# Kernel optimization log

Measured on AMD Instinct MI355X. Metric: run time of the kernel, lower is better.

The kernel has to match this reference:

```python
import jax, jax.numpy as jnp
import numpy as np

B, C, N, H = 4, 512, 2048, 8
D = C // H  # per-head depth = 64
EPS = 1e-5


def conv1x1(x, W, b):
    # x: [B, Cin, N], W: [Cout, Cin], b: [Cout]
    return jnp.einsum('oc,bcn->bon', W, x) + b[None, :, None]


def instance_norm(x):
    # normalize over length dim per (batch, channel), no affine
    mu = jnp.mean(x, axis=-1, keepdims=True)
    var = jnp.var(x, axis=-1, keepdims=True)
    return (x - mu) * jax.lax.rsqrt(var + EPS)


def _pipeline(src, tgt, Wq, bq, Wk, bk, Wv, bv, Wm, bm):
    # query from src, key/value from tgt; reshape C -> (D outer, H inner)
    q = conv1x1(src, Wq, bq).reshape(B, D, H, N)
    k = conv1x1(tgt, Wk, bk).reshape(B, D, H, N)
    v = conv1x1(tgt, Wv, bv).reshape(B, D, H, N)
    scores = jnp.einsum('bdhn,bdhm->bhnm', q, k) / jnp.sqrt(jnp.float32(D))
    probs = jax.nn.softmax(scores, axis=-1)
    out = jnp.einsum('bhnm,bdhm->bdhn', probs, v).reshape(B, C, N)
    return conv1x1(out, Wm, bm)


def _mlp(x, W1, b1, W2, b2):
    h = conv1x1(x, W1, b1)
    h = jax.nn.relu(instance_norm(h))
    return conv1x1(h, W2, b2)


def setup_inputs() -> dict:
    key = jax.random.key(0)
    ks = jax.random.split(key, 8)
    s = 0.02
    return {
        'source_features': jax.random.normal(ks[0], (B, C, N), jnp.float32),
        'target_features': jax.random.normal(ks[1], (B, C, N), jnp.float32),
        'Wq': jax.random.normal(ks[2], (C, C), jnp.float32) * s,
        'bq': jnp.zeros((C,), jnp.float32),
        'Wk': jax.random.normal(ks[3], (C, C), jnp.float32) * s,
        'bk': jnp.zeros((C,), jnp.float32),
        'Wv': jax.random.normal(ks[4], (C, C), jnp.float32) * s,
        'bv': jnp.zeros((C,), jnp.float32),
        'Wm': jax.random.normal(ks[5], (C, C), jnp.float32) * s,
        'bm': jnp.zeros((C,), jnp.float32),
        'W1': jax.random.normal(ks[6], (2 * C, 2 * C), jnp.float32) * s,
        'b1': jnp.zeros((2 * C,), jnp.float32),
        'W2': jax.random.normal(ks[7], (C, 2 * C), jnp.float32) * s,
        'b2': jnp.zeros((C,), jnp.float32),
    }


def reference(source_features, target_features, Wq, bq, Wk, bk, Wv, bv, Wm, bm, W1, b1, W2, b2):
    src, tgt = source_features, target_features
    # source update uses ORIGINAL target features
    src_att = _pipeline(src, tgt, Wq, bq, Wk, bk, Wv, bv, Wm, bm)
    src = src + _mlp(jnp.concatenate([src, src_att], axis=1), W1, b1, W2, b2)
    # target update uses the UPDATED source features (in-place semantics of original)
    tgt_att = _pipeline(tgt, src, Wq, bq, Wk, bk, Wv, bv, Wm, bm)
    tgt = tgt + _mlp(jnp.concatenate([tgt, tgt_att], axis=1), W1, b1, W2, b2)
    return src, tgt
```

## Files before the change

### kernel.cpp

```cpp
#include <hip/hip_runtime.h>

#define NN 2048
#define CC 512
#define BB 4
#define HH 8
#define DD 64
#define SCALE 0.18033688011112043f

typedef unsigned short u16;
typedef __attribute__((ext_vector_type(8))) short bf16x8;
typedef __attribute__((ext_vector_type(4))) float f32x4;

extern "C" __device__ float __ocml_native_exp2_f32(float);

__device__ inline u16 f2b(float x) {
    unsigned u = __builtin_bit_cast(unsigned, x);
    u += 0x7fffu + ((u >> 16) & 1u);
    return (u16)(u >> 16);
}
__device__ inline float b2f(u16 h) {
    unsigned u = ((unsigned)h) << 16;
    return __builtin_bit_cast(float, u);
}

#define GLD16(g, l) __builtin_amdgcn_global_load_lds( \
    (const __attribute__((address_space(1))) unsigned int*)(g), \
    (__attribute__((address_space(3))) unsigned int*)(l), 16, 0, 0)

template<int JT, bool DBUF>
__device__ __forceinline__ void gemm_core_t(
    const u16* __restrict__ Xa, const u16* __restrict__ Xb, int Ca, int K,
    const u16* __restrict__ Wt, size_t rowBase,
    u16* As, u16* Bs, f32x4 (&acc)[4][JT])
{
    constexpr int OT = JT * 32;
    constexpr int ASZ = 128 * 64, BSZ = OT * 64;
    const int tid = threadIdx.x;
    const int lane = tid & 63, w = tid >> 6;
    const int quad = lane >> 4, l16 = lane & 15;
    const int wrow = w & 1, wcol = w >> 1;
    const int arow = lane >> 3, aseg = lane & 7;
    const int asw = aseg ^ arow;
    const int lk = l16 & 7;

    auto stage = [&](int k0, u16* Ad, u16* Bd) {
        const u16* Xs; int Crow, cc;
        if (k0 < Ca) { Xs = Xa; Crow = Ca; cc = k0; }
        else         { Xs = Xb; Crow = K - Ca; cc = k0 - Ca; }
#pragma unroll
        for (int i = 0; i < 4; ++i) {
            int rl = w * 32 + i * 8 + arow;
            int la = __builtin_amdgcn_readfirstlane((w * 32 + i * 8) * 64);
            GLD16(Xs + (rowBase + rl) * (size_t)Crow + cc + asw * 8, (char*)Ad + (size_t)la * 2);
        }
#pragma unroll
        for (int i = 0; i < OT / 32; ++i) {
            int rl = w * (OT / 4) + i * 8 + arow;
            int la = __builtin_amdgcn_readfirstlane((w * (OT / 4) + i * 8) * 64);
            GLD16(Wt + (size_t)rl * K + k0 + asw * 8, (char*)Bd + (size_t)la * 2);
        }
    };
    auto compute = [&](const u16* Ac, const u16* Bc) {
#pragma unroll
        for (int kk = 0; kk < 2; ++kk) {
            const int g = ((kk * 4 + quad) ^ lk) * 8;
            bf16x8 av[4], bv[JT];
#pragma unroll
            for (int i = 0; i < 4; ++i)
                av[i] = *(const bf16x8*)&Ac[(wrow * 64 + i * 16 + l16) * 64 + g];
#pragma unroll
            for (int jj = 0; jj < JT; ++jj)
                bv[jj] = *(const bf16x8*)&Bc[(wcol * JT * 16 + jj * 16 + l16) * 64 + g];
#pragma unroll
            for (int i = 0; i < 4; ++i)
#pragma unroll
                for (int jj = 0; jj < JT; ++jj)
                    acc[i][jj] = __builtin_amdgcn_mfma_f32_16x16x32_bf16(av[i], bv[jj], acc[i][jj], 0, 0, 0);
        }
    };

    if constexpr (DBUF) {
        stage(0, As, Bs);
        const int nt = K / 64;
        for (int t = 0; t < nt; ++t) {
            const u16* Ac = As + (t & 1) * ASZ;
            const u16* Bc = Bs + (t & 1) * BSZ;
            __syncthreads();
            if (t + 1 < nt)
                stage((t + 1) * 64, As + ((t + 1) & 1) * ASZ, Bs + ((t + 1) & 1) * BSZ);
            compute(Ac, Bc);
        }
    } else {
        for (int k0 = 0; k0 < K; k0 += 64) {
            stage(k0, As, Bs);
            __syncthreads();
            compute(As, Bs);
            __syncthreads();
        }
    }
}

template<int JT>
__device__ __forceinline__ void gemm_epilogue_t(
    f32x4 (&acc)[4][JT], const float* __restrict__ bias, int mode,
    int b, int n0, int o0, int Cout,
    const float* __restrict__ res, float* __restrict__ outF, u16* __restrict__ outB)
{
    const int tid = threadIdx.x;
    const int lane = tid & 63, w = tid >> 6;
    const int quad = lane >> 4, l16 = lane & 15;
    const int wrow = w & 1, wcol = w >> 1;
    const size_t bN = (size_t)b * NN;
    const int nb0 = n0 + wrow * 64, ob0 = o0 + wcol * JT * 16;

    if (mode == 0) {
#pragma unroll
        for (int j = 0; j < JT; ++j) {
            int o = ob0 + j * 16 + l16;
            float bs = bias[o];
#pragma unroll
            for (int i = 0; i < 4; ++i)
#pragma unroll
                for (int r = 0; r < 4; ++r) {
                    int n = nb0 + i * 16 + quad * 4 + r;
                    outB[(bN + n) * Cout + o] = f2b(acc[i][j][r] + bs);
                }
        }
    } else if (mode == 1) {
#pragma unroll
        for (int j = 0; j < JT; ++j) {
            int o = ob0 + j * 16 + l16;
            float bs = bias[o];
            int h = o >> 6, d = o & 63;
#pragma unroll
            for (int i = 0; i < 4; ++i) {
                int n = nb0 + i * 16 + quad * 4;
                ushort4 pk;
                pk.x = f2b(acc[i][j][0] + bs); pk.y = f2b(acc[i][j][1] + bs);
                pk.z = f2b(acc[i][j][2] + bs); pk.w = f2b(acc[i][j][3] + bs);
                *(ushort4*)&outB[(((size_t)b * HH + h) * DD + d) * NN + n] = pk;
            }
        }
    } else {
#pragma unroll
        for (int j = 0; j < JT; ++j) {
            int o = ob0 + j * 16 + l16;
            float bs = bias[o];
#pragma unroll
            for (int i = 0; i < 4; ++i) {
                int n = nb0 + i * 16 + quad * 4;
                size_t ad = ((size_t)b * Cout + o) * NN + n;
                float4 rv = *(const float4*)&res[ad];
                float4 yv;
                yv.x = acc[i][j][0] + bs + rv.x;
                yv.y = acc[i][j][1] + bs + rv.y;
                yv.z = acc[i][j][2] + bs + rv.z;
                yv.w = acc[i][j][3] + bs + rv.w;
                *(float4*)&outF[ad] = yv;
                if (mode == 2) {
                    outB[(bN + n + 0) * Cout + o] = f2b(yv.x);
                    outB[(bN + n + 1) * Cout + o] = f2b(yv.y);
                    outB[(bN + n + 2) * Cout + o] = f2b(yv.z);
                    outB[(bN + n + 3) * Cout + o] = f2b(yv.w);
                }
            }
        }
    }
}

template<int JT>
__global__ __launch_bounds__(256, (JT == 2 ? 3 : 2)) void gemm_bf16_t(
    const u16* __restrict__ Wb, const float* __restrict__ bias,
    const u16* __restrict__ Xa, const u16* __restrict__ Xb,
    int Ca, int K, int Cout,
    const float* __restrict__ res, float* __restrict__ outF,
    u16* __restrict__ outB, int mode)
{
    __shared__ u16 As[2 * 128 * 64];
    __shared__ u16 Bs[2 * JT * 32 * 64];
    const int b = blockIdx.z, n0 = blockIdx.x * 128, o0 = blockIdx.y * (JT * 32);
    f32x4 acc[4][JT] = {};
    gemm_core_t<JT, true>(Xa, Xb, Ca, K, Wb + (size_t)o0 * K, (size_t)b * NN + n0, As, Bs, acc);
    gemm_epilogue_t<JT>(acc, bias, mode, b, n0, o0, Cout, res, outF, outB);
}

__global__ __launch_bounds__(256, 3) void gemm_qkv(
    const u16* __restrict__ WQ, const float* __restrict__ bQ,
    const u16* __restrict__ XQ, u16* __restrict__ outQ,
    const u16* __restrict__ WK, const float* __restrict__ bK, u16* __restrict__ outK,
    const u16* __restrict__ WV, const float* __restrict__ bV, u16* __restrict__ outV,
    const u16* __restrict__ XKV)
{
    __shared__ u16 As[128 * 64];
    __shared__ u16 Bs[128 * 64];
    const int yb = blockIdx.y;
    const u16* W; const float* bias; const u16* X; u16* outB; int mode, o0;
    if (yb < 4)      { o0 = yb * 128;       W = WQ; bias = bQ; X = XQ;  outB = outQ; mode = 0; }
    else if (yb < 8) { o0 = (yb - 4) * 128; W = WK; bias = bK; X = XKV; outB = outK; mode = 0; }
    else             { o0 = (yb - 8) * 128; W = WV; bias = bV; X = XKV; outB = outV; mode = 1; }
    const int b = blockIdx.z, n0 = blockIdx.x * 128;
    f32x4 acc[4][4] = {};
    gemm_core_t<4, false>(X, nullptr, 512, 512, W + (size_t)o0 * 512, (size_t)b * NN + n0, As, Bs, acc);
    gemm_epilogue_t<4>(acc, bias, mode, b, n0, o0, 512, nullptr, nullptr, outB);
}

__global__ __launch_bounds__(512, 4) void attn(
    const u16* __restrict__ Qg, const u16* __restrict__ Kg,
    const u16* __restrict__ Vg, u16* __restrict__ Og)
{
    __shared__ __align__(16) u16 pool[6 * 4096];
    u16* const Ksb[2] = { pool, pool + 4096 };
    u16* const Vtb[2] = { pool + 2 * 4096, pool + 3 * 4096 };
    u16* const Ps = pool + 4 * 4096;
    const int tid = threadIdx.x;
    const int lane = tid & 63, w = tid >> 6;
    const int qg = w & 3, hv = w >> 2;
    const int quad = lane >> 4, l16 = lane & 15;
    const int id = blockIdx.x;
    const int xcd = id & 7, jj = id >> 3;
    const int bh = xcd * 4 + (jj >> 4), nb = jj & 15;
    const int b = bh >> 3, h = bh & 7;
    const int n0 = nb * 128, wn0 = qg * 32;
    const int sr0 = w * 8;
    const size_t qkBase = ((size_t)b * NN) * CC + h * DD;
    const size_t vBase  = (((size_t)b * HH + h) * DD) * NN;
    const int r8 = lane >> 3, seg = lane & 7;
    const int segp = seg ^ r8;
    const int lk = l16 & 7;

    const u16* kp = Kg + qkBase + (size_t)(sr0 + r8) * CC + segp * 8;
    const u16* vp = Vg + vBase + (size_t)(sr0 + r8) * NN + segp * 8;

    bf16x8 qf[2][2];
#pragma unroll
    for (int qs = 0; qs < 2; ++qs) {
        int n = n0 + wn0 + qs * 16 + l16;
#pragma unroll
        for (int ks = 0; ks < 2; ++ks)
            qf[qs][ks] = *(const bf16x8*)&Qg[qkBase + (size_t)n * CC + ks * 32 + quad * 8];
    }

    const short oneb = 0x3F80;
    const bf16x8 ones = {oneb, oneb, oneb, oneb, oneb, oneb, oneb, oneb};
    f32x4 oa[2][4] = {};
    f32x4 lacc[2] = {};

    GLD16(kp, Ksb[0] + sr0 * 64);
    GLD16(vp, Vtb[0] + sr0 * 64);
    kp += 64 * CC; vp += 64;

#define ATTN_PREF(BUF) do { \
        GLD16(kp, Ksb[BUF] + sr0 * 64); \
        GLD16(vp, Vtb[BUF] + sr0 * 64); \
        kp += 64 * CC; vp += 64; \
    } while (0)

#define ATTN_BODY(CUR) do { \
        const u16* ksb = Ksb[CUR]; \
        const u16* vtb = Vtb[CUR]; \
        f32x4 st[2][2] = {}; \
        _Pragma("unroll") \
        for (int ks = 0; ks < 2; ++ks) { \
            bf16x8 ak[2]; \
            _Pragma("unroll") \
            for (int rtl = 0; rtl < 2; ++rtl) \
                ak[rtl] = *(const bf16x8*)&ksb[(hv * 32 + rtl * 16 + l16) * 64 + ((ks * 4 + quad) ^ lk) * 8]; \
            __builtin_amdgcn_s_setprio(1); \
            _Pragma("unroll") \
            for (int rtl = 0; rtl < 2; ++rtl) \
                _Pragma("unroll") \
                for (int qs = 0; qs < 2; ++qs) \
                    st[qs][rtl] = __builtin_amdgcn_mfma_f32_16x16x32_bf16(ak[rtl], qf[qs][ks], st[qs][rtl], 0, 0, 0); \
            __builtin_amdgcn_s_setprio(0); \
        } \
        _Pragma("unroll") \
        for (int qs = 0; qs < 2; ++qs) { \
            int nrow = wn0 + qs * 16 + l16; \
            _Pragma("unroll") \
            for (int rtl = 0; rtl < 2; ++rtl) { \
                unsigned u0 = __builtin_bit_cast(unsigned, __ocml_native_exp2_f32(st[qs][rtl][0])); \
                unsigned u1 = __builtin_bit_cast(unsigned, __ocml_native_exp2_f32(st[qs][rtl][1])); \
                unsigned u2 = __builtin_bit_cast(unsigned, __ocml_native_exp2_f32(st[qs][rtl][2])); \
                unsigned u3 = __builtin_bit_cast(unsigned, __ocml_native_exp2_f32(st[qs][rtl][3])); \
                uint2 t; \
                t.x = __builtin_amdgcn_perm(u1, u0, 0x07060302u); \
                t.y = __builtin_amdgcn_perm(u3, u2, 0x07060302u); \
                int g = (((hv * 2 + rtl) * 2 + (quad >> 1))) ^ lk; \
                *(uint2*)&Ps[nrow * 64 + g * 8 + (quad & 1) * 4] = t; \
            } \
        } \
        { \
            bf16x8 pa[2]; \
            _Pragma("unroll") \
            for (int qs = 0; qs < 2; ++qs) \
                pa[qs] = *(const bf16x8*)&Ps[(wn0 + qs * 16 + l16) * 64 + ((hv * 4 + quad) ^ lk) * 8]; \
            bf16x8 vb[4]; \
            _Pragma("unroll") \
            for (int ct = 0; ct < 4; ++ct) \
                vb[ct] = *(const bf16x8*)&vtb[(ct * 16 + l16) * 64 + ((hv * 4 + quad) ^ lk) * 8]; \
            __builtin_amdgcn_s_setprio(1); \
            _Pragma("unroll") \
            for (int ct = 0; ct < 4; ++ct) \
                _Pragma("unroll") \
                for (int qs = 0; qs < 2; ++qs) \
                    oa[qs][ct] = __builtin_amdgcn_mfma_f32_16x16x32_bf16(pa[qs], vb[ct], oa[qs][ct], 0, 0, 0); \
            _Pragma("unroll") \
            for (int qs = 0; qs < 2; ++qs) \
                lacc[qs] = __builtin_amdgcn_mfma_f32_16x16x32_bf16(pa[qs], ones, lacc[qs], 0, 0, 0); \
            __builtin_amdgcn_s_setprio(0); \
        } \
    } while (0)

    for (int it = 0; it < NN / 64; it += 2) {
        __syncthreads();
        ATTN_PREF(1);
        ATTN_BODY(0);
        __syncthreads();
        if (it < NN / 64 - 2)
            ATTN_PREF(0);
        ATTN_BODY(1);
    }
#undef ATTN_PREF
#undef ATTN_BODY

    __syncthreads();
    float* M = (float*)pool;
    const int mbase = (qg * 64 + lane) * 41;
    if (hv == 1) {
#pragma unroll
        for (int qs = 0; qs < 2; ++qs)
#pragma unroll
            for (int ct = 0; ct < 4; ++ct)
                *(f32x4*)&M[mbase + (qs * 4 + ct) * 4] = oa[qs][ct];
        *(f32x4*)&M[mbase + 32] = lacc[0];
        *(f32x4*)&M[mbase + 36] = lacc[1];
    }
    __syncthreads();
    if (hv == 0) {
#pragma unroll
        for (int qs = 0; qs < 2; ++qs)
#pragma unroll
            for (int ct = 0; ct < 4; ++ct)
                oa[qs][ct] += *(const f32x4*)&M[mbase + (qs * 4 + ct) * 4];
        lacc[0] += *(const f32x4*)&M[mbase + 32];
        lacc[1] += *(const f32x4*)&M[mbase + 36];
#pragma unroll
        for (int qs = 0; qs < 2; ++qs)
#pragma unroll
            for (int r = 0; r < 4; ++r) {
                float li = 1.f / lacc[qs][r];
                int n = n0 + wn0 + qs * 16 + quad * 4 + r;
#pragma unroll
                for (int ct = 0; ct < 4; ++ct)
                    Og[qkBase + (size_t)n * CC + ct * 16 + l16] = f2b(oa[qs][ct][r] * li);
            }
    }
}

__global__ __launch_bounds__(256) void transpose_cvt(
    const float* __restrict__ X, u16* __restrict__ Y)
{
    __shared__ float T[64][65];
    const int tid = threadIdx.x;
    const int n0 = blockIdx.x * 64, c0 = blockIdx.y * 64, b = blockIdx.z;
    const int rr = tid >> 4, cc4 = tid & 15;
#pragma unroll
    for (int p = 0; p < 4; ++p) {
        int cl = p * 16 + rr;
        float4 v = *(const float4*)&X[((size_t)b * CC + c0 + cl) * NN + n0 + cc4 * 4];
        T[cl][cc4 * 4 + 0] = v.x; T[cl][cc4 * 4 + 1] = v.y;
        T[cl][cc4 * 4 + 2] = v.z; T[cl][cc4 * 4 + 3] = v.w;
    }
    __syncthreads();
#pragma unroll
    for (int p = 0; p < 4; ++p) {
        int nl = p * 16 + rr;
        ushort4 pk;
        pk.x = f2b(T[cc4 * 4 + 0][nl]);
        pk.y = f2b(T[cc4 * 4 + 1][nl]);
        pk.z = f2b(T[cc4 * 4 + 2][nl]);
        pk.w = f2b(T[cc4 * 4 + 3][nl]);
        *(ushort4*)&Y[((size_t)b * NN + n0 + nl) * CC + c0 + cc4 * 4] = pk;
    }
}

__global__ __launch_bounds__(256) void prep_weights(
    const float* __restrict__ Wq, const float* __restrict__ Wk,
    const float* __restrict__ Wv, const float* __restrict__ Wm,
    const float* __restrict__ W1, const float* __restrict__ W2,
    u16* oQ, u16* oK, u16* oV, u16* oM, u16* o1, u16* o2)
{
    const float* W; u16* o; int rows, cols, perm; float sc = 1.f;
    switch (blockIdx.z) {
        case 0: W = Wq; o = oQ; rows = 512;  cols = 512;  perm = 1; sc = SCALE; break;
        case 1: W = Wk; o = oK; rows = 512;  cols = 512;  perm = 1; break;
        case 2: W = Wv; o = oV; rows = 512;  cols = 512;  perm = 1; break;
        case 3: W = Wm; o = oM; rows = 512;  cols = 512;  perm = 2; break;
        case 4: W = W1; o = o1; rows = 1024; cols = 1024; perm = 0; break;
        default: W = W2; o = o2; rows = 512; cols = 1024; perm = 0; break;
    }
    int c = blockIdx.x * 256 + threadIdx.x;
    int r = blockIdx.y;
    if (r >= rows || c >= cols) return;
    int sr = r, scol = c;
    if (perm == 1) sr = (r & 63) * 8 + (r >> 6);
    else if (perm == 2) scol = (c & 63) * 8 + (c >> 6);
    o[(size_t)r * cols + c] = f2b(W[(size_t)sr * cols + scol] * sc);
}

__global__ void prep_bias(const float* __restrict__ bq, const float* __restrict__ bk,
                          const float* __restrict__ bv,
                          float* oq, float* ok, float* ov)
{
    int i = blockIdx.x * 256 + threadIdx.x;
    int y = blockIdx.y;
    const float* s = (y == 0) ? bq : (y == 1) ? bk : bv;
    float* o = (y == 0) ? oq : (y == 1) ? ok : ov;
    float v = s[(i & 63) * 8 + (i >> 6)];
    if (y == 0) v *= SCALE;
    o[i] = v;
}

__global__ __launch_bounds__(256) void inorm_p1(
    const u16* __restrict__ X, float* __restrict__ Ssum, float* __restrict__ Ssq)
{
    __shared__ float rs[4][64], rq[4][64];
    const int tid = threadIdx.x;
    const int cl = tid & 63, g = tid >> 6;
    const int c = blockIdx.x * 64 + cl;
    const int b = blockIdx.y, nz = blockIdx.z;
    float s = 0.f, q = 0.f;
    size_t base = ((size_t)b * NN + nz * 256 + g * 64) * 1024 + c;
#pragma unroll 4
    for (int i = 0; i < 64; ++i) {
        float x = b2f(X[base + (size_t)i * 1024]);
        s += x; q += x * x;
    }
    rs[g][cl] = s; rq[g][cl] = q;
    __syncthreads();
    if (g == 0) {
        s = rs[0][cl] + rs[1][cl] + rs[2][cl] + rs[3][cl];
        q = rq[0][cl] + rq[1][cl] + rq[2][cl] + rq[3][cl];
        atomicAdd(&Ssum[b * 1024 + c], s);
        atomicAdd(&Ssq[b * 1024 + c], q);
    }
}

__global__ __launch_bounds__(256) void inorm_p2(
    u16* __restrict__ X, const float* __restrict__ Ssum, const float* __restrict__ Ssq)
{
    const int tid = threadIdx.x;
    const int cl = tid & 63, g = tid >> 6;
    const int c = blockIdx.x * 64 + cl;
    const int b = blockIdx.y, nz = blockIdx.z;
    float mean = Ssum[b * 1024 + c] * (1.f / NN);
    float var  = Ssq[b * 1024 + c] * (1.f / NN) - mean * mean;
    float rstd = rsqrtf(fmaxf(var, 0.f) + 1e-5f);
    size_t base = ((size_t)b * NN + nz * 256 + g * 64) * 1024 + c;
#pragma unroll 4
    for (int i = 0; i < 64; ++i) {
        float x = b2f(X[base + (size_t)i * 1024]);
        x = (x - mean) * rstd;
        X[base + (size_t)i * 1024] = f2b(fmaxf(x, 0.f));
    }
}

extern "C" void kernel_launch(void* const* d_in, const int* in_sizes, int n_in,
                              void* d_out, int out_size, void* d_ws, size_t ws_size,
                              hipStream_t stream)
{
    (void)in_sizes; (void)n_in; (void)out_size; (void)ws_size;
    const float* src = (const float*)d_in[0];
    const float* tgt = (const float*)d_in[1];
    const float* Wq = (const float*)d_in[2];  const float* bq = (const float*)d_in[3];
    const float* Wk = (const float*)d_in[4];  const float* bk = (const float*)d_in[5];
    const float* Wv = (const float*)d_in[6];  const float* bv = (const float*)d_in[7];
    const float* Wm = (const float*)d_in[8];  const float* bm = (const float*)d_in[9];
    const float* W1 = (const float*)d_in[10]; const float* b1 = (const float*)d_in[11];
    const float* W2 = (const float*)d_in[12]; const float* b2 = (const float*)d_in[13];

    char* w = (char*)d_ws;
    u16* WQp = (u16*)(w);
    u16* WKp = (u16*)(w + (512u << 10));
    u16* WVp = (u16*)(w + (1u << 20));
    u16* WMp = (u16*)(w + (3u << 19));
    u16* W1b = (u16*)(w + (2u << 20));
    u16* W2b = (u16*)(w + (4u << 20));
    float* BQp = (float*)(w + (5u << 20));
    float* BKp = BQp + 512;
    float* BVp = BQp + 1024;
    float* STS = BQp + 1536;
    float* STQ = STS + 4096;
    u16* X0 = (u16*)(w + ( 6u << 20));
    u16* X1 = (u16*)(w + (14u << 20));
    u16* B0 = (u16*)(w + (22u << 20));
    u16* B1 = (u16*)(w + (30u << 20));
    u16* B2 = (u16*)(w + (38u << 20));
    u16* B3 = (u16*)(w + (46u << 20));

    float* out = (float*)d_out;
    const size_t R = (size_t)BB * CC * NN;
    dim3 blk(256), blkA(512);

    prep_weights<<<dim3(4, 1024, 6), blk, 0, stream>>>(Wq, Wk, Wv, Wm, W1, W2,
                                                       WQp, WKp, WVp, WMp, W1b, W2b);
    prep_bias<<<dim3(2, 3), blk, 0, stream>>>(bq, bk, bv, BQp, BKp, BVp);
    transpose_cvt<<<dim3(32, 8, 4), blk, 0, stream>>>(src, X0);
    transpose_cvt<<<dim3(32, 8, 4), blk, 0, stream>>>(tgt, X1);

    dim3 gQKV(16, 12, 4), gM(16, 8, 4), gW1(16, 8, 4), gW2(16, 8, 4);

    gemm_qkv<<<gQKV, blk, 0, stream>>>(WQp, BQp, X0, B0, WKp, BKp, B1, WVp, BVp, B2, X1);
    attn<<<dim3(512), blkA, 0, stream>>>(B0, B1, B2, B3);
    gemm_bf16_t<2><<<gM, blk, 0, stream>>>(WMp, bm, B3, nullptr, 512, 512, 512, nullptr, nullptr, B0, 0);
    gemm_bf16_t<4><<<gW1, blk, 0, stream>>>(W1b, b1, X0, B0, 512, 1024, 1024, nullptr, nullptr, B1, 0);
    hipMemsetAsync(STS, 0, 8192 * sizeof(float), stream);
    inorm_p1<<<dim3(16, 4, 8), blk, 0, stream>>>(B1, STS, STQ);
    inorm_p2<<<dim3(16, 4, 8), blk, 0, stream>>>(B1, STS, STQ);
    gemm_bf16_t<2><<<gW2, blk, 0, stream>>>(W2b, b2, B1, nullptr, 1024, 1024, 512, src, out, B3, 2);

    gemm_qkv<<<gQKV, blk, 0, stream>>>(WQp, BQp, X1, X0, WKp, BKp, B0, WVp, BVp, B1, B3);
    attn<<<dim3(512), blkA, 0, stream>>>(X0, B0, B1, B2);
    gemm_bf16_t<2><<<gM, blk, 0, stream>>>(WMp, bm, B2, nullptr, 512, 512, 512, nullptr, nullptr, X0, 0);
    gemm_bf16_t<4><<<gW1, blk, 0, stream>>>(W1b, b1, X1, X0, 512, 1024, 1024, nullptr, nullptr, B0, 0);
    hipMemsetAsync(STS, 0, 8192 * sizeof(float), stream);
    inorm_p1<<<dim3(16, 4, 8), blk, 0, stream>>>(B0, STS, STQ);
    inorm_p2<<<dim3(16, 4, 8), blk, 0, stream>>>(B0, STS, STQ);
    gemm_bf16_t<2><<<gW2, blk, 0, stream>>>(W2b, b2, B0, nullptr, 1024, 1024, 512, tgt, out + R, nullptr, 3);
}
```

Baseline: 401.8 us.

## Use 512-thread double-buffered GEMM for QKV and W1 projections

Adds a new GEMM core and epilogue that split each 128x128 output tile across 8 waves (4x2 accumulators per wave) with double-buffered shared memory staging. The QKV and W1 projections now run on this path at 512 threads per block. This is meant to raise occupancy and overlap global loads with MFMA work. The other GEMMs get launch bounds of 3, and the attention reduction scratch stride moves from 41 to 44, likely to align the vector stores. The cost is more shared memory per block and possible register pressure.

```diff
diff --git a/kernel.cpp b/kernel.cpp
--- a/kernel.cpp
+++ b/kernel.cpp
@@ -169,7 +169,7 @@
 }
 
 template<int JT>
-__global__ __launch_bounds__(256, (JT == 2 ? 3 : 2)) void gemm_bf16_t(
+__global__ __launch_bounds__(256, 3) void gemm_bf16_t(
     const u16* __restrict__ Wb, const float* __restrict__ bias,
     const u16* __restrict__ Xa, const u16* __restrict__ Xb,
     int Ca, int K, int Cout,
@@ -184,24 +184,146 @@
     gemm_epilogue_t<JT>(acc, bias, mode, b, n0, o0, Cout, res, outF, outB);
 }
 
-__global__ __launch_bounds__(256, 3) void gemm_qkv(
+template<bool DBUF>
+__device__ __forceinline__ void gemm_core8(
+    const u16* __restrict__ Xa, const u16* __restrict__ Xb, int Ca, int K,
+    const u16* __restrict__ Wt, size_t rowBase,
+    u16* As, u16* Bs, f32x4 (&acc)[4][2])
+{
+    constexpr int ASZ = 128 * 64, BSZ = 128 * 64;
+    const int tid = threadIdx.x;
+    const int lane = tid & 63, w = tid >> 6;
+    const int quad = lane >> 4, l16 = lane & 15;
+    const int wr = w & 1, wc = w >> 1;
+    const int arow = lane >> 3, aseg = lane & 7;
+    const int asw = aseg ^ arow;
+    const int lk = l16 & 7;
+
+    auto stage = [&](int k0, u16* Ad, u16* Bd) {
+        const u16* Xs; int Crow, cc;
+        if (k0 < Ca) { Xs = Xa; Crow = Ca; cc = k0; }
+        else         { Xs = Xb; Crow = K - Ca; cc = k0 - Ca; }
+#pragma unroll
+        for (int i = 0; i < 2; ++i) {
+            int rl = w * 16 + i * 8 + arow;
+            int la = __builtin_amdgcn_readfirstlane((w * 16 + i * 8) * 64);
+            GLD16(Xs + (rowBase + rl) * (size_t)Crow + cc + asw * 8, (char*)Ad + (size_t)la * 2);
+            GLD16(Wt + (size_t)rl * K + k0 + asw * 8, (char*)Bd + (size_t)la * 2);
+        }
+    };
+    auto compute = [&](const u16* Ac, const u16* Bc) {
+#pragma unroll
+        for (int kk = 0; kk < 2; ++kk) {
+            const int g = ((kk * 4 + quad) ^ lk) * 8;
+            bf16x8 av[4], bv[2];
+#pragma unroll
+            for (int i = 0; i < 4; ++i)
+                av[i] = *(const bf16x8*)&Ac[(wr * 64 + i * 16 + l16) * 64 + g];
+#pragma unroll
+            for (int j = 0; j < 2; ++j)
+                bv[j] = *(const bf16x8*)&Bc[(wc * 32 + j * 16 + l16) * 64 + g];
+#pragma unroll
+            for (int i = 0; i < 4; ++i)
+#pragma unroll
+                for (int j = 0; j < 2; ++j)
+                    acc[i][j] = __builtin_amdgcn_mfma_f32_16x16x32_bf16(av[i], bv[j], acc[i][j], 0, 0, 0);
+        }
+    };
+
+    if constexpr (DBUF) {
+        stage(0, As, Bs);
+        const int nt = K / 64;
+        for (int t = 0; t < nt; ++t) {
+            const u16* Ac = As + (t & 1) * ASZ;
+            const u16* Bc = Bs + (t & 1) * BSZ;
+            __syncthreads();
+            if (t + 1 < nt)
+                stage((t + 1) * 64, As + ((t + 1) & 1) * ASZ, Bs + ((t + 1) & 1) * BSZ);
+            compute(Ac, Bc);
+        }
+    } else {
+        for (int k0 = 0; k0 < K; k0 += 64) {
+            stage(k0, As, Bs);
+            __syncthreads();
+            compute(As, Bs);
+            __syncthreads();
+        }
+    }
+}
+
+__device__ __forceinline__ void gemm_epilogue8(
+    f32x4 (&acc)[4][2], const float* __restrict__ bias, int mode,
+    int b, int n0, int o0, int Cout, u16* __restrict__ outB)
+{
+    const int tid = threadIdx.x;
+    const int lane = tid & 63, w = tid >> 6;
+    const int quad = lane >> 4, l16 = lane & 15;
+    const int wr = w & 1, wc = w >> 1;
+    const size_t bN = (size_t)b * NN;
+    const int nb0 = n0 + wr * 64, ob0 = o0 + wc * 32;
+
+    if (mode == 0) {
+#pragma unroll
+        for (int j = 0; j < 2; ++j) {
+            int o = ob0 + j * 16 + l16;
+            float bs = bias[o];
+#pragma unroll
+            for (int i = 0; i < 4; ++i)
+#pragma unroll
+                for (int r = 0; r < 4; ++r) {
+                    int n = nb0 + i * 16 + quad * 4 + r;
+                    outB[(bN + n) * Cout + o] = f2b(acc[i][j][r] + bs);
+                }
+        }
+    } else {
+#pragma unroll
+        for (int j = 0; j < 2; ++j) {
+            int o = ob0 + j * 16 + l16;
+            float bs = bias[o];
+            int h = o >> 6, d = o & 63;
+#pragma unroll
+            for (int i = 0; i < 4; ++i) {
+                int n = nb0 + i * 16 + quad * 4;
+                ushort4 pk;
+                pk.x = f2b(acc[i][j][0] + bs); pk.y = f2b(acc[i][j][1] + bs);
+                pk.z = f2b(acc[i][j][2] + bs); pk.w = f2b(acc[i][j][3] + bs);
+                *(ushort4*)&outB[(((size_t)b * HH + h) * DD + d) * NN + n] = pk;
+            }
+        }
+    }
+}
+
+__global__ __launch_bounds__(512, 4) void gemm_qkv(
     const u16* __restrict__ WQ, const float* __restrict__ bQ,
     const u16* __restrict__ XQ, u16* __restrict__ outQ,
     const u16* __restrict__ WK, const float* __restrict__ bK, u16* __restrict__ outK,
     const u16* __restrict__ WV, const float* __restrict__ bV, u16* __restrict__ outV,
     const u16* __restrict__ XKV)
 {
-    __shared__ u16 As[128 * 64];
-    __shared__ u16 Bs[128 * 64];
+    __shared__ u16 As[2 * 128 * 64];
+    __shared__ u16 Bs[2 * 128 * 64];
     const int yb = blockIdx.y;
     const u16* W; const float* bias; const u16* X; u16* outB; int mode, o0;
     if (yb < 4)      { o0 = yb * 128;       W = WQ; bias = bQ; X = XQ;  outB = outQ; mode = 0; }
     else if (yb < 8) { o0 = (yb - 4) * 128; W = WK; bias = bK; X = XKV; outB = outK; mode = 0; }
     else             { o0 = (yb - 8) * 128; W = WV; bias = bV; X = XKV; outB = outV; mode = 1; }
     const int b = blockIdx.z, n0 = blockIdx.x * 128;
-    f32x4 acc[4][4] = {};
-    gemm_core_t<4, false>(X, nullptr, 512, 512, W + (size_t)o0 * 512, (size_t)b * NN + n0, As, Bs, acc);
-    gemm_epilogue_t<4>(acc, bias, mode, b, n0, o0, 512, nullptr, nullptr, outB);
+    f32x4 acc[4][2] = {};
+    gemm_core8<true>(X, nullptr, 512, 512, W + (size_t)o0 * 512, (size_t)b * NN + n0, As, Bs, acc);
+    gemm_epilogue8(acc, bias, mode, b, n0, o0, 512, outB);
+}
+
+__global__ __launch_bounds__(512, 4) void gemm_w1(
+    const u16* __restrict__ Wb, const float* __restrict__ bias,
+    const u16* __restrict__ Xa, const u16* __restrict__ Xb,
+    u16* __restrict__ outB)
+{
+    __shared__ u16 As[2 * 128 * 64];
+    __shared__ u16 Bs[2 * 128 * 64];
+    const int b = blockIdx.z, n0 = blockIdx.x * 128, o0 = blockIdx.y * 128;
+    f32x4 acc[4][2] = {};
+    gemm_core8<true>(Xa, Xb, 512, 1024, Wb + (size_t)o0 * 1024, (size_t)b * NN + n0, As, Bs, acc);
+    gemm_epilogue8(acc, bias, 0, b, n0, o0, 1024, outB);
 }
 
 __global__ __launch_bounds__(512, 4) void attn(
@@ -325,7 +447,7 @@
 
     __syncthreads();
     float* M = (float*)pool;
-    const int mbase = (qg * 64 + lane) * 41;
+    const int mbase = (qg * 64 + lane) * 44;
     if (hv == 1) {
 #pragma unroll
         for (int qs = 0; qs < 2; ++qs)
@@ -510,19 +632,19 @@
 
     dim3 gQKV(16, 12, 4), gM(16, 8, 4), gW1(16, 8, 4), gW2(16, 8, 4);
 
-    gemm_qkv<<<gQKV, blk, 0, stream>>>(WQp, BQp, X0, B0, WKp, BKp, B1, WVp, BVp, B2, X1);
+    gemm_qkv<<<gQKV, blkA, 0, stream>>>(WQp, BQp, X0, B0, WKp, BKp, B1, WVp, BVp, B2, X1);
     attn<<<dim3(512), blkA, 0, stream>>>(B0, B1, B2, B3);
     gemm_bf16_t<2><<<gM, blk, 0, stream>>>(WMp, bm, B3, nullptr, 512, 512, 512, nullptr, nullptr, B0, 0);
-    gemm_bf16_t<4><<<gW1, blk, 0, stream>>>(W1b, b1, X0, B0, 512, 1024, 1024, nullptr, nullptr, B1, 0);
+    gemm_w1<<<gW1, blkA, 0, stream>>>(W1b, b1, X0, B0, B1);
     hipMemsetAsync(STS, 0, 8192 * sizeof(float), stream);
     inorm_p1<<<dim3(16, 4, 8), blk, 0, stream>>>(B1, STS, STQ);
     inorm_p2<<<dim3(16, 4, 8), blk, 0, stream>>>(B1, STS, STQ);
     gemm_bf16_t<2><<<gW2, blk, 0, stream>>>(W2b, b2, B1, nullptr, 1024, 1024, 512, src, out, B3, 2);
 
-    gemm_qkv<<<gQKV, blk, 0, stream>>>(WQp, BQp, X1, X0, WKp, BKp, B0, WVp, BVp, B1, B3);
+    gemm_qkv<<<gQKV, blkA, 0, stream>>>(WQp, BQp, X1, X0, WKp, BKp, B0, WVp, BVp, B1, B3);
     attn<<<dim3(512), blkA, 0, stream>>>(X0, B0, B1, B2);
     gemm_bf16_t<2><<<gM, blk, 0, stream>>>(WMp, bm, B2, nullptr, 512, 512, 512, nullptr, nullptr, X0, 0);
-    gemm_bf16_t<4><<<gW1, blk, 0, stream>>>(W1b, b1, X1, X0, 512, 1024, 1024, nullptr, nullptr, B0, 0);
+    gemm_w1<<<gW1, blkA, 0, stream>>>(W1b, b1, X1, X0, B0);
     hipMemsetAsync(STS, 0, 8192 * sizeof(float), stream);
     inorm_p1<<<dim3(16, 4, 8), blk, 0, stream>>>(B0, STS, STQ);
     inorm_p2<<<dim3(16, 4, 8), blk, 0, stream>>>(B0, STS, STQ);
```

Result: no change. 397.1 us (-1.2%).
